# Kernel optimization log

Hardware: AMD Instinct MI355X
Metric: run time of the kernel (lower is better)

The kernel has to match this reference:

```python
import jax, jax.numpy as jnp
import numpy as np

SYMMETRIC = True
NORMED = True

# (distance, angle) -> pixel offsets (row, col) exactly as in the original:
# row = round(sin(angle))*d, col = round(cos(angle))*d for angles 0, pi/4, pi/2, 3pi/4
OFFSETS = [(0, 1), (1, 1), (1, 0), (1, -1),
           (0, 2), (2, 2), (2, 0), (2, -2),
           (0, 3), (3, 3), (3, 0), (3, -3)]


def setup_inputs() -> dict:
    key = jax.random.key(0)
    inputs = jax.random.normal(key, (128, 512, 512, 1), dtype=jnp.float32)
    return {"inputs": inputs}


def _glcm_one(img, row, col):
    # img: binarized [B,H,W,C]
    B, H, W, C = img.shape
    if col > 0:
        a = img[:, :H - row, :W - col, :]
        b = img[:, row:, col:, :]
    else:
        # -0 slice == full width, matching the original Keras code
        a = img[:, :H - row, -col:, :]
        b = img[:, row:, :W + col, :]
    axes = (1, 2, 3)
    a_or_b = jnp.maximum(a, b)
    a_and_b = a * b
    M00 = jnp.sum(1.0 - a_or_b, axis=axes)           # [B]
    M01 = jnp.sum(b * (1.0 - a), axis=axes)
    M10 = jnp.sum(a * (1.0 - b), axis=axes)
    M11 = jnp.sum(a_and_b, axis=axes)
    if SYMMETRIC:
        temp = jnp.stack([M00 * 2.0, M01 + M10, M01 + M10, M11 * 2.0], axis=1)  # [B,4]
    else:
        temp = jnp.stack([M00, M01, M10, M11], axis=1)
    if NORMED:
        temp = temp / jnp.sum(temp, axis=1, keepdims=True)
    return temp


def reference(inputs) -> jnp.ndarray:
    # Binarize once (original redundantly re-binarizes per glcm pass; same math).
    img = jnp.sign(inputs)
    outs = [_glcm_one(img, r, c) for (r, c) in OFFSETS]
    return jnp.concatenate(outs, axis=1)  # [B, 48]
```

## Files before the change

### kernel.cpp

```cpp
#include <hip/hip_runtime.h>
#include <stdint.h>

#define BATCH 128
#define HH 512
#define WW 512
#define BAND 64
#define NB (HH / BAND)
#define HALO 3
#define PITCH 10

__device__ __forceinline__ uint32_t popc8(const uint64_t* R) {
    uint32_t s = 0;
#pragma unroll
    for (int w = 0; w < 8; ++w) s += (uint32_t)__popcll(R[w]);
    return s;
}

__device__ __forceinline__ void shiftdn(const uint64_t* R, const int sh, uint64_t* S) {
#pragma unroll
    for (int t8 = 0; t8 < 2; ++t8)
#pragma unroll
        for (int k = 0; k < 4; ++k) {
            int kc = k + sh;
            if (kc < 4) {
                S[t8 * 4 + k] = R[t8 * 4 + kc];
            } else {
                uint64_t x = R[t8 * 4 + kc - 4] >> 1;
                if (t8 == 0) x |= R[4 + kc - 4] << 63;
                S[t8 * 4 + k] = x;
            }
        }
}

__device__ __forceinline__ void procC(const uint64_t* A, const uint64_t* B, const int c,
                                      uint32_t* acc) {
    const int sh = c > 0 ? c : -c;
    uint64_t S[8];
    uint32_t oa = 0, ob = 0, on = 0;
    if (c > 0) {
        shiftdn(B, sh, S);
#pragma unroll
        for (int w = 0; w < 8; ++w) {
            uint64_t a = A[w];
            uint64_t am = ((w >> 2) == 1 && (w & 3) >= 4 - sh) ? (a & ~(1ull << 63)) : a;
            oa += (uint32_t)__popcll(am);
            ob += (uint32_t)__popcll(S[w]);
            on += (uint32_t)__popcll(a & S[w]);
        }
    } else {
        shiftdn(A, sh, S);
#pragma unroll
        for (int w = 0; w < 8; ++w) {
            uint64_t bb = B[w];
            uint64_t bm = ((w >> 2) == 1 && (w & 3) >= 4 - sh) ? (bb & ~(1ull << 63)) : bb;
            oa += (uint32_t)__popcll(S[w]);
            ob += (uint32_t)__popcll(bm);
            on += (uint32_t)__popcll(S[w] & bb);
        }
    }
    acc[0] += oa; acc[1] += ob; acc[2] += on;
}

__device__ __forceinline__ void proc0(const uint64_t* A, const uint64_t* B,
                                      uint32_t rpA, uint32_t rpB, uint32_t* acc) {
    uint32_t on = 0;
#pragma unroll
    for (int w = 0; w < 8; ++w) on += (uint32_t)__popcll(A[w] & B[w]);
    acc[0] += rpA; acc[1] += rpB; acc[2] += on;
}

__device__ __forceinline__ void loadrow(const uint64_t* lds, int y, uint64_t* R) {
#pragma unroll
    for (int i = 0; i < 4; ++i)
        *(ulonglong2*)&R[2 * i] = *(const ulonglong2*)&lds[y * PITCH + 2 * i];
}

__device__ __forceinline__ float4 ldtask(const float* base, int y0, int id, int lane) {
    int row = id >> 1, half = id & 1;
    return *(const float4*)(base + (size_t)(y0 + row) * WW + half * 256 + lane * 4);
}

__device__ __forceinline__ void balstore(uint64_t* lds, int id, float4 v, int lane) {
    uint64_t m0 = __ballot(v.x < 0.f);
    uint64_t m1 = __ballot(v.y < 0.f);
    uint64_t m2 = __ballot(v.z < 0.f);
    uint64_t m3 = __ballot(v.w < 0.f);
    if (lane == 0) {
        int row = id >> 1, half = id & 1;
        uint64_t* p = &lds[row * PITCH + half * 4];
        ulonglong2 s0, s1;
        s0.x = m0; s0.y = m1; s1.x = m2; s1.y = m3;
        *(ulonglong2*)&p[0] = s0;
        *(ulonglong2*)&p[2] = s1;
    }
}

__global__ __launch_bounds__(256) void glcm_fused(const float* __restrict__ img,
                                                  uint32_t* __restrict__ part) {
    __shared__ uint64_t lds[(BAND + HALO) * PITCH];
    int blk = (int)blockIdx.x;
    int band = blk & (NB - 1);
    int b = blk >> 3;
    int y0 = band * BAND;
    int t = (int)threadIdx.x, lane = t & 63, wv = t >> 6;
    const float* base = img + (size_t)b * HH * WW;

    int nrows = min(BAND + HALO, HH - y0);
    int ntasks = nrows * 2;

    int id = wv;
    for (; id + 12 < ntasks; id += 16) {
        float4 v0 = ldtask(base, y0, id, lane);
        float4 v1 = ldtask(base, y0, id + 4, lane);
        float4 v2 = ldtask(base, y0, id + 8, lane);
        float4 v3 = ldtask(base, y0, id + 12, lane);
        balstore(lds, id, v0, lane);
        balstore(lds, id + 4, v1, lane);
        balstore(lds, id + 8, v2, lane);
        balstore(lds, id + 12, v3, lane);
    }
    for (; id < ntasks; id += 4) {
        float4 v = ldtask(base, y0, id, lane);
        balstore(lds, id, v, lane);
    }
    __syncthreads();

    uint32_t acc[3][3];
#pragma unroll
    for (int o = 0; o < 3; ++o) { acc[o][0] = 0; acc[o][1] = 0; acc[o][2] = 0; }

    int r = lane;
    uint64_t A[8];
    loadrow(lds, r, A);

    if (wv == 0) {
        procC(A, A, 1, acc[0]);
        procC(A, A, 2, acc[1]);
        procC(A, A, 3, acc[2]);
    } else if (wv == 1) {
        if (y0 + r + 1 < HH) {
            uint64_t B[8];
            loadrow(lds, r + 1, B);
            uint32_t rpA = popc8(A), rpB = popc8(B);
            procC(A, B, 1, acc[0]);
            proc0(A, B, rpA, rpB, acc[1]);
            procC(A, B, -1, acc[2]);
        }
    } else if (wv == 2) {
        if (y0 + r + 2 < HH) {
            uint64_t B[8];
            loadrow(lds, r + 2, B);
            uint32_t rpA = popc8(A), rpB = popc8(B);
            procC(A, B, 2, acc[0]);
            proc0(A, B, rpA, rpB, acc[1]);
            procC(A, B, -2, acc[2]);
        }
    } else {
        if (y0 + r + 3 < HH) {
            uint64_t B[8];
            loadrow(lds, r + 3, B);
            uint32_t rpA = popc8(A), rpB = popc8(B);
            procC(A, B, 3, acc[0]);
            proc0(A, B, rpA, rpB, acc[1]);
            procC(A, B, -3, acc[2]);
        }
    }

#pragma unroll
    for (int o = 0; o < 3; ++o)
#pragma unroll
        for (int q = 0; q < 3; ++q) {
            int v = (int)acc[o][q];
            for (int m = 32; m >= 1; m >>= 1) v += __shfl_xor(v, m, 64);
            acc[o][q] = (uint32_t)v;
        }
    if (lane == 0) {
        const int jt[4][3] = {{0, 4, 8}, {1, 2, 3}, {5, 6, 7}, {9, 10, 11}};
        uint32_t* pb = part + (size_t)blk * 36;
#pragma unroll
        for (int o = 0; o < 3; ++o)
#pragma unroll
            for (int q = 0; q < 3; ++q) pb[jt[wv][o] * 3 + q] = acc[o][q];
    }
}

__global__ __launch_bounds__(64) void glcm_final(const uint32_t* __restrict__ part,
                                                 float* __restrict__ out) {
    __shared__ uint32_t sums[36];
    int b = (int)blockIdx.x;
    int t = (int)threadIdx.x;
    if (t < 36) {
        uint32_t s = 0;
        const uint32_t* p = part + (size_t)b * NB * 36 + t;
#pragma unroll
        for (int k = 0; k < NB; ++k) s += p[k * 36];
        sums[t] = s;
    }
    __syncthreads();
    if (t < 12) {
        const int rtab[12] = {0, 1, 1, 1, 0, 2, 2, 2, 0, 3, 3, 3};
        const int ctab[12] = {1, 1, 0, -1, 2, 2, 0, -2, 3, 3, 0, -3};
        int r = rtab[t];
        int sh = ctab[t] < 0 ? -ctab[t] : ctab[t];
        float foa = (float)sums[t * 3 + 0];
        float fob = (float)sums[t * 3 + 1];
        float fon = (float)sums[t * 3 + 2];
        float Nwin = (float)((HH - r) * (WW - sh));
        float e0 = 4.f * fon;
        float e1 = 2.f * (foa + fob) - 8.f * fon;
        float e3 = 2.f * Nwin - 4.f * (foa + fob) + 8.f * fon;
        float inv = 1.0f / (2.f * Nwin - 4.f * fon);
        float4 o;
        o.x = e0 * inv; o.y = e1 * inv; o.z = e1 * inv; o.w = e3 * inv;
        *(float4*)(out + (size_t)b * 48 + t * 4) = o;
    }
}

extern "C" void kernel_launch(void* const* d_in, const int* in_sizes, int n_in,
                              void* d_out, int out_size, void* d_ws, size_t ws_size,
                              hipStream_t stream) {
    const float* img = (const float*)d_in[0];
    float* out = (float*)d_out;
    uint32_t* part = (uint32_t*)d_ws;
    (void)in_sizes; (void)n_in; (void)out_size; (void)ws_size;

    glcm_fused<<<dim3(BATCH * NB), dim3(256), 0, stream>>>(img, part);
    glcm_final<<<dim3(BATCH), dim3(64), 0, stream>>>(part, out);
}
```

Before: 30.85 us.

## Fuse final reduction into main kernel via per-band flag spin-wait

Removes the second launch. Band-0 blocks now spin-wait on release flags set by the other seven band blocks of the same image, then sum the partials and write the normalized outputs. The flags are reset afterwards for reuse. Launch bounds gain a min-blocks hint of 4. This saves a kernel launch and its gap, but depends on the other band blocks being co-resident or scheduled so the spinning band-0 blocks cannot deadlock, and on the workspace flags starting at zero.

```diff
diff --git a/kernel.cpp b/kernel.cpp
--- a/kernel.cpp
+++ b/kernel.cpp
@@ -8,6 +8,7 @@
 #define NB (HH / BAND)
 #define HALO 3
 #define PITCH 10
+#define MAGIC 0x5F3C9D21u
 
 __device__ __forceinline__ uint32_t popc8(const uint64_t* R) {
     uint32_t s = 0;
@@ -95,8 +96,10 @@
     }
 }
 
-__global__ __launch_bounds__(256) void glcm_fused(const float* __restrict__ img,
-                                                  uint32_t* __restrict__ part) {
+__global__ __launch_bounds__(256, 4) void glcm_fused(const float* __restrict__ img,
+                                                     uint32_t* __restrict__ part,
+                                                     uint32_t* __restrict__ flags,
+                                                     float* __restrict__ out) {
     __shared__ uint64_t lds[(BAND + HALO) * PITCH];
     int blk = (int)blockIdx.x;
     int band = blk & (NB - 1);
@@ -182,38 +185,48 @@
 #pragma unroll
             for (int q = 0; q < 3; ++q) pb[jt[wv][o] * 3 + q] = acc[o][q];
     }
-}
-
-__global__ __launch_bounds__(64) void glcm_final(const uint32_t* __restrict__ part,
-                                                 float* __restrict__ out) {
-    __shared__ uint32_t sums[36];
-    int b = (int)blockIdx.x;
-    int t = (int)threadIdx.x;
-    if (t < 36) {
-        uint32_t s = 0;
-        const uint32_t* p = part + (size_t)b * NB * 36 + t;
-#pragma unroll
-        for (int k = 0; k < NB; ++k) s += p[k * 36];
-        sums[t] = s;
-    }
     __syncthreads();
-    if (t < 12) {
+
+    if (band != 0) {
+        if (t == 0) {
+            __threadfence();
+            __hip_atomic_store(&flags[blk], MAGIC, __ATOMIC_RELEASE, __HIP_MEMORY_SCOPE_AGENT);
+        }
+        return;
+    }
+
+    if (wv != 0) return;
+    if (lane >= 1 && lane < NB) {
+        while (__hip_atomic_load(&flags[blk + lane], __ATOMIC_ACQUIRE,
+                                 __HIP_MEMORY_SCOPE_AGENT) != MAGIC)
+            __builtin_amdgcn_s_sleep(2);
+    }
+    __threadfence();
+
+    if (lane < 12) {
         const int rtab[12] = {0, 1, 1, 1, 0, 2, 2, 2, 0, 3, 3, 3};
         const int ctab[12] = {1, 1, 0, -1, 2, 2, 0, -2, 3, 3, 0, -3};
-        int r = rtab[t];
-        int sh = ctab[t] < 0 ? -ctab[t] : ctab[t];
-        float foa = (float)sums[t * 3 + 0];
-        float fob = (float)sums[t * 3 + 1];
-        float fon = (float)sums[t * 3 + 2];
-        float Nwin = (float)((HH - r) * (WW - sh));
+        uint32_t oa = 0, ob = 0, on = 0;
+        for (int k = 0; k < NB; ++k) {
+            const uint32_t* p = part + (size_t)(blk + k) * 36 + lane * 3;
+            oa += __hip_atomic_load(&p[0], __ATOMIC_RELAXED, __HIP_MEMORY_SCOPE_AGENT);
+            ob += __hip_atomic_load(&p[1], __ATOMIC_RELAXED, __HIP_MEMORY_SCOPE_AGENT);
+            on += __hip_atomic_load(&p[2], __ATOMIC_RELAXED, __HIP_MEMORY_SCOPE_AGENT);
+        }
+        int rr = rtab[lane];
+        int sh = ctab[lane] < 0 ? -ctab[lane] : ctab[lane];
+        float foa = (float)oa, fob = (float)ob, fon = (float)on;
+        float Nwin = (float)((HH - rr) * (WW - sh));
         float e0 = 4.f * fon;
         float e1 = 2.f * (foa + fob) - 8.f * fon;
         float e3 = 2.f * Nwin - 4.f * (foa + fob) + 8.f * fon;
         float inv = 1.0f / (2.f * Nwin - 4.f * fon);
         float4 o;
         o.x = e0 * inv; o.y = e1 * inv; o.z = e1 * inv; o.w = e3 * inv;
-        *(float4*)(out + (size_t)b * 48 + t * 4) = o;
-    }
+        *(float4*)(out + (size_t)b * 48 + lane * 4) = o;
+    }
+    if (lane >= 1 && lane < NB)
+        __hip_atomic_store(&flags[blk + lane], 0u, __ATOMIC_RELEASE, __HIP_MEMORY_SCOPE_AGENT);
 }
 
 extern "C" void kernel_launch(void* const* d_in, const int* in_sizes, int n_in,
@@ -222,8 +235,8 @@
     const float* img = (const float*)d_in[0];
     float* out = (float*)d_out;
     uint32_t* part = (uint32_t*)d_ws;
+    uint32_t* flags = (uint32_t*)d_ws + BATCH * NB * 36;
     (void)in_sizes; (void)n_in; (void)out_size; (void)ws_size;
 
-    glcm_fused<<<dim3(BATCH * NB), dim3(256), 0, stream>>>(img, part);
-    glcm_final<<<dim3(BATCH), dim3(64), 0, stream>>>(part, out);
-}
+    glcm_fused<<<dim3(BATCH * NB), dim3(256), 0, stream>>>(img, part, flags, out);
+}
```

Result: slower. 85.73 us (+177.9%).
